# Performance work log

Measured on AMD Instinct MI355X. Metric: run time of the kernel, lower is better.

## Reference

```python
import jax, jax.numpy as jnp
import numpy as np

IN_C, OUT_C, K, STRIDE, PAD, N_EXPERTS = 64, 128, 3, 1, 1, 4
B, H, W = 32, 64, 64


def setup_inputs() -> dict:
    key = jax.random.key(0)
    k1, k2, k3, k4 = jax.random.split(key, 4)
    x = jax.random.normal(k1, (B, IN_C, H, W), dtype=jnp.float32)
    idx = jax.random.randint(k2, (B,), 0, N_EXPERTS, dtype=jnp.int64)
    # Expert conv weights/biases (PyTorch Conv2d layout: [out_c, in_c, kh, kw])
    fan_in = IN_C * K * K
    bound = 1.0 / np.sqrt(fan_in)
    Wc = jax.random.uniform(k3, (N_EXPERTS, OUT_C, IN_C, K, K), dtype=jnp.float32,
                            minval=-bound, maxval=bound)
    bc = jax.random.uniform(k4, (N_EXPERTS, OUT_C), dtype=jnp.float32,
                            minval=-bound, maxval=bound)
    return {"x": x, "idx": idx, "Wc": Wc, "bc": bc}


def _conv2d(x, w, b):
    # x: [B, C_in, H, W], w: [C_out, C_in, K, K], b: [C_out]
    y = jax.lax.conv_general_dilated(
        x, w,
        window_strides=(STRIDE, STRIDE),
        padding=[(PAD, PAD), (PAD, PAD)],
        dimension_numbers=("NCHW", "OIHW", "NCHW"),
    )
    return y + b[None, :, None, None]


def reference(x, idx, Wc, bc):
    # Compute every expert's conv for every sample (faithful to the torch code),
    # then gather each sample's selected expert output.
    results = jax.vmap(lambda w, b: _conv2d(x, w, b))(Wc, bc)  # [E, B, C_out, H, W]
    results = jnp.moveaxis(results, 0, 1)                      # [B, E, C_out, H, W]
    out = jnp.take_along_axis(
        results, idx[:, None, None, None, None].astype(jnp.int32), axis=1
    )  # [B, 1, C_out, H, W]
    return jnp.squeeze(out, axis=1)
```

## Files before the change

### kernel.cpp

```cpp
#include <hip/hip_runtime.h>
#include <hip/hip_bf16.h>


#define IC 64
#define OC 128
#define HH 64
#define WW 64

typedef short short8 __attribute__((ext_vector_type(8)));
typedef ushort ushort8 __attribute__((ext_vector_type(8)));
typedef float float16 __attribute__((ext_vector_type(16)));

typedef const __attribute__((address_space(1))) void gas_t;
typedef __attribute__((address_space(3))) void las_t;

static __device__ __forceinline__ ushort f2bf(float v) {
    __hip_bfloat16 h = __float2bfloat16(v);
    return *(ushort*)&h;
}

__global__ __launch_bounds__(256)
void reorder_w(const float* __restrict__ Wc, ushort* __restrict__ wout) {
    __shared__ ushort lw[4 * 584];
    const int t   = threadIdx.x;
    const int e   = blockIdx.x >> 5;
    const int oc0 = (blockIdx.x & 31) * 4;
    const float* src = Wc + (size_t)(e * 128 + oc0) * 576;
#pragma unroll
    for (int k = 0; k < 9; ++k) {
        const int f   = k * 256 + t;
        const int ocl = f / 576;
        const int rem = f - ocl * 576;
        lw[ocl * 584 + rem] = f2bf(src[f]);
    }
    __syncthreads();
#pragma unroll
    for (int k = 0; k < 2; ++k) {
        const int n = k * 256 + t;
        if (n < 288) {
            const int ocl = n & 3, ich = (n >> 2) & 7, tap = n >> 5;
            ushort8 v;
#pragma unroll
            for (int icl = 0; icl < 8; ++icl)
                v[icl] = lw[ocl * 584 + (ich * 8 + icl) * 9 + tap];
            *(ushort8*)(wout +
                ((((size_t)(e * 9 + tap) * 8 + ich) * 128 + oc0 + ocl) * 8)) = v;
        }
    }
}

__global__ __launch_bounds__(256, 4)
void moe_conv_mfma(const float* __restrict__ x, const int* __restrict__ idx,
                   const ushort* __restrict__ wre, const float* __restrict__ bc,
                   float* __restrict__ out) {
    __shared__ __align__(16) ushort xs[4 * 8 * 66 * 8];
    __shared__ __align__(16) ushort wbuf[2][8192];
    __shared__ float bias[128];

    const int t = threadIdx.x;

    const int lin = blockIdx.x;
    const int nw  = (lin & 7) * 128 + (lin >> 3);
    const int b   = nw >> 5;
    const int rp  = nw & 31;
    const int row0 = rp * 2;
    const int e    = ((unsigned)idx[b]) & 3;

    const int lane31 = t & 31;
    const int lane64 = t & 63;
    const int lhi    = (t >> 5) & 1;
    const int wv     = t >> 6;
    const int w0     = wv & 1;
    const int pr     = wv >> 1;

    const ushort* we = wre + (size_t)e * 9 * 8192;

#pragma unroll
    for (int i = 0; i < 4; ++i) {
        __builtin_amdgcn_global_load_lds(
            (gas_t*)(we + wv * 2048 + i * 512 + lane64 * 8),
            (las_t*)&wbuf[0][wv * 2048 + i * 512], 16, 0, 0);
    }

    if (t < 128) {
        const int r = t >> 5, rem = t & 31;
        const int ich = rem >> 2, side = (rem >> 1) & 1, q = rem & 1;
        const int hc = side ? 65 : 0;
        ushort4 z = {0, 0, 0, 0};
        *(ushort4*)&xs[(((r * 8 + ich) * 66 + hc) * 8 + q * 4)] = z;
    } else {
        bias[t - 128] = bc[e * OC + (t - 128)];
    }

    const float* xb = x + (size_t)b * IC * HH * WW;
    {
        const int gc   = t & 63;
        const int csel = t >> 6;
#pragma unroll
        for (int it = 0; it < 16; ++it) {
            const int combo = it * 4 + csel;
            const int r = combo >> 4, rem = combo & 15;
            const int ich = rem >> 1, q = rem & 1;
            const int gr = row0 - 1 + r;
            ushort4 u = {0, 0, 0, 0};
            if ((unsigned)gr < (unsigned)HH) {
                const int ic0 = ich * 8 + q * 4;
                u.x = f2bf(xb[((ic0 + 0) * HH + gr) * WW + gc]);
                u.y = f2bf(xb[((ic0 + 1) * HH + gr) * WW + gc]);
                u.z = f2bf(xb[((ic0 + 2) * HH + gr) * WW + gc]);
                u.w = f2bf(xb[((ic0 + 3) * HH + gr) * WW + gc]);
            }
            *(ushort4*)&xs[(((r * 8 + ich) * 66 + (gc + 1)) * 8 + q * 4)] = u;
        }
    }

    float16 acc[2][2];
#pragma unroll
    for (int a = 0; a < 2; ++a)
#pragma unroll
        for (int cg = 0; cg < 2; ++cg)
#pragma unroll
            for (int r = 0; r < 16; ++r) acc[a][cg][r] = 0.0f;

    const int xbase = ((pr * 8 + lhi) * 66 + lane31) * 8;

#pragma unroll
    for (int tap = 0; tap < 9; ++tap) {
        const int cur = tap & 1;
        if (tap < 8) {
            const ushort* wt = we + (tap + 1) * 8192;
#pragma unroll
            for (int i = 0; i < 4; ++i) {
                __builtin_amdgcn_global_load_lds(
                    (gas_t*)(wt + wv * 2048 + i * 512 + lane64 * 8),
                    (las_t*)&wbuf[cur ^ 1][wv * 2048 + i * 512], 16, 0, 0);
            }
            asm volatile("s_waitcnt vmcnt(4) lgkmcnt(0)" ::: "memory");
        } else {
            asm volatile("s_waitcnt vmcnt(0) lgkmcnt(0)" ::: "memory");
        }
        __builtin_amdgcn_s_barrier();

        const int kh = tap / 3;
        const int kw = tap - kh * 3;
        const int off = ((kh * 8) * 66 + kw) * 8;

        __builtin_amdgcn_s_setprio(1);
#pragma unroll
        for (int ks = 0; ks < 4; ++ks) {
            const int ich = ks * 2 + lhi;
            const short8 a0 = *(const short8*)&wbuf[cur][(ich * 128 + w0 * 64 + lane31) * 8];
            const short8 a1 = *(const short8*)&wbuf[cur][(ich * 128 + w0 * 64 + 32 + lane31) * 8];
            const short8 b0 = *(const short8*)&xs[xbase + off + ks * 2 * 66 * 8];
            const short8 b1 = *(const short8*)&xs[xbase + off + ks * 2 * 66 * 8 + 256];
            acc[0][0] = __builtin_amdgcn_mfma_f32_32x32x16_bf16(a0, b0, acc[0][0], 0, 0, 0);
            acc[0][1] = __builtin_amdgcn_mfma_f32_32x32x16_bf16(a0, b1, acc[0][1], 0, 0, 0);
            acc[1][0] = __builtin_amdgcn_mfma_f32_32x32x16_bf16(a1, b0, acc[1][0], 0, 0, 0);
            acc[1][1] = __builtin_amdgcn_mfma_f32_32x32x16_bf16(a1, b1, acc[1][1], 0, 0, 0);
        }
        __builtin_amdgcn_s_setprio(0);

        __builtin_amdgcn_s_barrier();
    }

#pragma unroll
    for (int a = 0; a < 2; ++a) {
        const int ocb = w0 * 64 + a * 32 + 4 * lhi;
#pragma unroll
        for (int reg = 0; reg < 16; ++reg) {
            const int oc = ocb + (reg & 3) + 8 * (reg >> 2);
            const float bv = bias[oc];
            const size_t base = (((size_t)b * OC + oc) * HH + (row0 + pr)) * WW;
            out[base + lane31]      = acc[a][0][reg] + bv;
            out[base + 32 + lane31] = acc[a][1][reg] + bv;
        }
    }
}

extern "C" void kernel_launch(void* const* d_in, const int* in_sizes, int n_in,
                              void* d_out, int out_size, void* d_ws, size_t ws_size,
                              hipStream_t stream) {
    const float* x   = (const float*)d_in[0];
    const int*   idx = (const int*)d_in[1];
    const float* Wc  = (const float*)d_in[2];
    const float* bc  = (const float*)d_in[3];
    float* out  = (float*)d_out;
    ushort* wre = (ushort*)d_ws;

    reorder_w<<<128, 256, 0, stream>>>(Wc, wre);
    moe_conv_mfma<<<1024, 256, 0, stream>>>(x, idx, wre, bc, out);
}
```

Baseline: 120.0 us.

## Enlarge conv tile to 8 output rows per 512-thread block with full OC per wave

Each block now computes 8 output rows with 8 waves, each wave covering all 128 output channels for one row, instead of 2 rows with 4 waves splitting the channels. The input halo shrinks relative to useful rows (10 staged rows for 8 outputs instead of 4 for 2), and each weight tap loaded into LDS is reused across four times as many output rows. This cuts redundant x loads and bf16 conversion as well as weight traffic. In exchange it doubles accumulator registers per wave, uses more LDS, and launches only 256 blocks, which lowers occupancy and may underfill the GPU's CUs.

```diff
diff --git a/kernel.cpp b/kernel.cpp
--- a/kernel.cpp
+++ b/kernel.cpp
@@ -49,47 +49,44 @@
     }
 }
 
-__global__ __launch_bounds__(256, 4)
+__global__ __launch_bounds__(512, 2)
 void moe_conv_mfma(const float* __restrict__ x, const int* __restrict__ idx,
                    const ushort* __restrict__ wre, const float* __restrict__ bc,
                    float* __restrict__ out) {
-    __shared__ __align__(16) ushort xs[4 * 8 * 66 * 8];
+    __shared__ __align__(16) ushort xs[10 * 8 * 66 * 8];
     __shared__ __align__(16) ushort wbuf[2][8192];
     __shared__ float bias[128];
 
     const int t = threadIdx.x;
 
     const int lin = blockIdx.x;
-    const int nw  = (lin & 7) * 128 + (lin >> 3);
-    const int b   = nw >> 5;
-    const int rp  = nw & 31;
-    const int row0 = rp * 2;
+    const int nw  = (lin & 7) * 32 + (lin >> 3);
+    const int b   = nw >> 3;
+    const int rq  = nw & 7;
+    const int row0 = rq * 8;
     const int e    = ((unsigned)idx[b]) & 3;
 
     const int lane31 = t & 31;
-    const int lane64 = t & 63;
     const int lhi    = (t >> 5) & 1;
     const int wv     = t >> 6;
-    const int w0     = wv & 1;
-    const int pr     = wv >> 1;
 
     const ushort* we = wre + (size_t)e * 9 * 8192;
 
 #pragma unroll
-    for (int i = 0; i < 4; ++i) {
+    for (int i = 0; i < 2; ++i) {
         __builtin_amdgcn_global_load_lds(
-            (gas_t*)(we + wv * 2048 + i * 512 + lane64 * 8),
-            (las_t*)&wbuf[0][wv * 2048 + i * 512], 16, 0, 0);
+            (gas_t*)(we + i * 4096 + t * 8),
+            (las_t*)&wbuf[0][i * 4096 + t * 8], 16, 0, 0);
     }
 
-    if (t < 128) {
+    if (t < 320) {
         const int r = t >> 5, rem = t & 31;
         const int ich = rem >> 2, side = (rem >> 1) & 1, q = rem & 1;
         const int hc = side ? 65 : 0;
         ushort4 z = {0, 0, 0, 0};
         *(ushort4*)&xs[(((r * 8 + ich) * 66 + hc) * 8 + q * 4)] = z;
-    } else {
-        bias[t - 128] = bc[e * OC + (t - 128)];
+    } else if (t < 448) {
+        bias[t - 320] = bc[e * OC + (t - 320)];
     }
 
     const float* xb = x + (size_t)b * IC * HH * WW;
@@ -97,8 +94,8 @@
         const int gc   = t & 63;
         const int csel = t >> 6;
 #pragma unroll
-        for (int it = 0; it < 16; ++it) {
-            const int combo = it * 4 + csel;
+        for (int it = 0; it < 20; ++it) {
+            const int combo = it * 8 + csel;
             const int r = combo >> 4, rem = combo & 15;
             const int ich = rem >> 1, q = rem & 1;
             const int gr = row0 - 1 + r;
@@ -114,15 +111,16 @@
         }
     }
 
-    float16 acc[2][2];
+    float16 acc[4][2];
 #pragma unroll
-    for (int a = 0; a < 2; ++a)
+    for (int g = 0; g < 4; ++g)
 #pragma unroll
         for (int cg = 0; cg < 2; ++cg)
 #pragma unroll
-            for (int r = 0; r < 16; ++r) acc[a][cg][r] = 0.0f;
+            for (int r = 0; r < 16; ++r) acc[g][cg][r] = 0.0f;
 
-    const int xbase = ((pr * 8 + lhi) * 66 + lane31) * 8;
+    const int xrow  = wv * 4224 + lane31 * 8;
+    const int abase = lane31 * 8;
 
 #pragma unroll
     for (int tap = 0; tap < 9; ++tap) {
@@ -130,12 +128,12 @@
         if (tap < 8) {
             const ushort* wt = we + (tap + 1) * 8192;
 #pragma unroll
-            for (int i = 0; i < 4; ++i) {
+            for (int i = 0; i < 2; ++i) {
                 __builtin_amdgcn_global_load_lds(
-                    (gas_t*)(wt + wv * 2048 + i * 512 + lane64 * 8),
-                    (las_t*)&wbuf[cur ^ 1][wv * 2048 + i * 512], 16, 0, 0);
+                    (gas_t*)(wt + i * 4096 + t * 8),
+                    (las_t*)&wbuf[cur ^ 1][i * 4096 + t * 8], 16, 0, 0);
             }
-            asm volatile("s_waitcnt vmcnt(4) lgkmcnt(0)" ::: "memory");
+            asm volatile("s_waitcnt vmcnt(2) lgkmcnt(0)" ::: "memory");
         } else {
             asm volatile("s_waitcnt vmcnt(0) lgkmcnt(0)" ::: "memory");
         }
@@ -143,36 +141,45 @@
 
         const int kh = tap / 3;
         const int kw = tap - kh * 3;
-        const int off = ((kh * 8) * 66 + kw) * 8;
+        const int xtap = xrow + kh * 4224 + kw * 8;
 
         __builtin_amdgcn_s_setprio(1);
 #pragma unroll
         for (int ks = 0; ks < 4; ++ks) {
             const int ich = ks * 2 + lhi;
-            const short8 a0 = *(const short8*)&wbuf[cur][(ich * 128 + w0 * 64 + lane31) * 8];
-            const short8 a1 = *(const short8*)&wbuf[cur][(ich * 128 + w0 * 64 + 32 + lane31) * 8];
-            const short8 b0 = *(const short8*)&xs[xbase + off + ks * 2 * 66 * 8];
-            const short8 b1 = *(const short8*)&xs[xbase + off + ks * 2 * 66 * 8 + 256];
+            const int xo = xtap + ich * 528;
+            const short8 b0 = *(const short8*)&xs[xo];
+            const short8 b1 = *(const short8*)&xs[xo + 256];
+            const int ao = abase + ich * 1024;
+            const short8 a0 = *(const short8*)&wbuf[cur][ao];
+            const short8 a1 = *(const short8*)&wbuf[cur][ao + 256];
+            const short8 a2 = *(const short8*)&wbuf[cur][ao + 512];
+            const short8 a3 = *(const short8*)&wbuf[cur][ao + 768];
             acc[0][0] = __builtin_amdgcn_mfma_f32_32x32x16_bf16(a0, b0, acc[0][0], 0, 0, 0);
             acc[0][1] = __builtin_amdgcn_mfma_f32_32x32x16_bf16(a0, b1, acc[0][1], 0, 0, 0);
             acc[1][0] = __builtin_amdgcn_mfma_f32_32x32x16_bf16(a1, b0, acc[1][0], 0, 0, 0);
             acc[1][1] = __builtin_amdgcn_mfma_f32_32x32x16_bf16(a1, b1, acc[1][1], 0, 0, 0);
+            acc[2][0] = __builtin_amdgcn_mfma_f32_32x32x16_bf16(a2, b0, acc[2][0], 0, 0, 0);
+            acc[2][1] = __builtin_amdgcn_mfma_f32_32x32x16_bf16(a2, b1, acc[2][1], 0, 0, 0);
+            acc[3][0] = __builtin_amdgcn_mfma_f32_32x32x16_bf16(a3, b0, acc[3][0], 0, 0, 0);
+            acc[3][1] = __builtin_amdgcn_mfma_f32_32x32x16_bf16(a3, b1, acc[3][1], 0, 0, 0);
         }
         __builtin_amdgcn_s_setprio(0);
 
-        __builtin_amdgcn_s_barrier();
+        if (tap < 8)
+            __builtin_amdgcn_s_barrier();
     }
 
 #pragma unroll
-    for (int a = 0; a < 2; ++a) {
-        const int ocb = w0 * 64 + a * 32 + 4 * lhi;
+    for (int g = 0; g < 4; ++g) {
+        const int ocb = g * 32 + 4 * lhi;
 #pragma unroll
         for (int reg = 0; reg < 16; ++reg) {
             const int oc = ocb + (reg & 3) + 8 * (reg >> 2);
             const float bv = bias[oc];
-            const size_t base = (((size_t)b * OC + oc) * HH + (row0 + pr)) * WW;
-            out[base + lane31]      = acc[a][0][reg] + bv;
-            out[base + 32 + lane31] = acc[a][1][reg] + bv;
+            const size_t base = (((size_t)b * OC + oc) * HH + (row0 + wv)) * WW;
+            out[base + lane31]      = acc[g][0][reg] + bv;
+            out[base + 32 + lane31] = acc[g][1][reg] + bv;
         }
     }
 }
@@ -188,5 +195,5 @@
     ushort* wre = (ushort*)d_ws;
 
     reorder_w<<<128, 256, 0, stream>>>(Wc, wre);
-    moe_conv_mfma<<<1024, 256, 0, stream>>>(x, idx, wre, bc, out);
+    moe_conv_mfma<<<256, 512, 0, stream>>>(x, idx, wre, bc, out);
 }
```

After: 112.2 us. 6.5% less time.

## Enlarge conv tile to four output rows per 512-thread block, single-buffer weights

Applied to the files above, without the earlier changes.

Each block now computes four output rows with eight waves instead of two rows with four waves. This cuts redundant input-halo loads and halves per-row weight fetches. The weight buffer becomes single-buffered, with the next tap's load issued after the compute barrier, to keep LDS use about the same despite the larger input tile. The cost is losing overlap between weight loads and MFMA work within a block.

```diff
diff --git a/kernel.cpp b/kernel.cpp
--- a/kernel.cpp
+++ b/kernel.cpp
@@ -49,25 +49,24 @@
     }
 }
 
-__global__ __launch_bounds__(256, 4)
+__global__ __launch_bounds__(512, 4)
 void moe_conv_mfma(const float* __restrict__ x, const int* __restrict__ idx,
                    const ushort* __restrict__ wre, const float* __restrict__ bc,
                    float* __restrict__ out) {
-    __shared__ __align__(16) ushort xs[4 * 8 * 66 * 8];
-    __shared__ __align__(16) ushort wbuf[2][8192];
+    __shared__ __align__(16) ushort xs[6 * 8 * 66 * 8];
+    __shared__ __align__(16) ushort wbuf[8192];
     __shared__ float bias[128];
 
     const int t = threadIdx.x;
 
     const int lin = blockIdx.x;
-    const int nw  = (lin & 7) * 128 + (lin >> 3);
-    const int b   = nw >> 5;
-    const int rp  = nw & 31;
-    const int row0 = rp * 2;
+    const int nw  = (lin & 7) * 64 + (lin >> 3);
+    const int b   = nw >> 4;
+    const int rq  = nw & 15;
+    const int row0 = rq * 4;
     const int e    = ((unsigned)idx[b]) & 3;
 
     const int lane31 = t & 31;
-    const int lane64 = t & 63;
     const int lhi    = (t >> 5) & 1;
     const int wv     = t >> 6;
     const int w0     = wv & 1;
@@ -76,20 +75,20 @@
     const ushort* we = wre + (size_t)e * 9 * 8192;
 
 #pragma unroll
-    for (int i = 0; i < 4; ++i) {
+    for (int i = 0; i < 2; ++i) {
         __builtin_amdgcn_global_load_lds(
-            (gas_t*)(we + wv * 2048 + i * 512 + lane64 * 8),
-            (las_t*)&wbuf[0][wv * 2048 + i * 512], 16, 0, 0);
+            (gas_t*)(we + i * 4096 + t * 8),
+            (las_t*)&wbuf[i * 4096 + t * 8], 16, 0, 0);
     }
 
-    if (t < 128) {
+    if (t < 192) {
         const int r = t >> 5, rem = t & 31;
         const int ich = rem >> 2, side = (rem >> 1) & 1, q = rem & 1;
         const int hc = side ? 65 : 0;
         ushort4 z = {0, 0, 0, 0};
         *(ushort4*)&xs[(((r * 8 + ich) * 66 + hc) * 8 + q * 4)] = z;
-    } else {
-        bias[t - 128] = bc[e * OC + (t - 128)];
+    } else if (t < 320) {
+        bias[t - 192] = bc[e * OC + (t - 192)];
     }
 
     const float* xb = x + (size_t)b * IC * HH * WW;
@@ -97,8 +96,8 @@
         const int gc   = t & 63;
         const int csel = t >> 6;
 #pragma unroll
-        for (int it = 0; it < 16; ++it) {
-            const int combo = it * 4 + csel;
+        for (int it = 0; it < 12; ++it) {
+            const int combo = it * 8 + csel;
             const int r = combo >> 4, rem = combo & 15;
             const int ich = rem >> 1, q = rem & 1;
             const int gr = row0 - 1 + r;
@@ -122,37 +121,24 @@
 #pragma unroll
             for (int r = 0; r < 16; ++r) acc[a][cg][r] = 0.0f;
 
-    const int xbase = ((pr * 8 + lhi) * 66 + lane31) * 8;
-
 #pragma unroll
     for (int tap = 0; tap < 9; ++tap) {
-        const int cur = tap & 1;
-        if (tap < 8) {
-            const ushort* wt = we + (tap + 1) * 8192;
-#pragma unroll
-            for (int i = 0; i < 4; ++i) {
-                __builtin_amdgcn_global_load_lds(
-                    (gas_t*)(wt + wv * 2048 + i * 512 + lane64 * 8),
-                    (las_t*)&wbuf[cur ^ 1][wv * 2048 + i * 512], 16, 0, 0);
-            }
-            asm volatile("s_waitcnt vmcnt(4) lgkmcnt(0)" ::: "memory");
-        } else {
-            asm volatile("s_waitcnt vmcnt(0) lgkmcnt(0)" ::: "memory");
-        }
+        asm volatile("s_waitcnt vmcnt(0) lgkmcnt(0)" ::: "memory");
         __builtin_amdgcn_s_barrier();
 
         const int kh = tap / 3;
         const int kw = tap - kh * 3;
-        const int off = ((kh * 8) * 66 + kw) * 8;
+        const int rr = pr + kh;
+        const int hb = lane31 + kw;
 
         __builtin_amdgcn_s_setprio(1);
 #pragma unroll
         for (int ks = 0; ks < 4; ++ks) {
             const int ich = ks * 2 + lhi;
-            const short8 a0 = *(const short8*)&wbuf[cur][(ich * 128 + w0 * 64 + lane31) * 8];
-            const short8 a1 = *(const short8*)&wbuf[cur][(ich * 128 + w0 * 64 + 32 + lane31) * 8];
-            const short8 b0 = *(const short8*)&xs[xbase + off + ks * 2 * 66 * 8];
-            const short8 b1 = *(const short8*)&xs[xbase + off + ks * 2 * 66 * 8 + 256];
+            const short8 a0 = *(const short8*)&wbuf[(ich * 128 + w0 * 64 + lane31) * 8];
+            const short8 a1 = *(const short8*)&wbuf[(ich * 128 + w0 * 64 + 32 + lane31) * 8];
+            const short8 b0 = *(const short8*)&xs[((rr * 8 + ich) * 66 + hb) * 8];
+            const short8 b1 = *(const short8*)&xs[((rr * 8 + ich) * 66 + hb + 32) * 8];
             acc[0][0] = __builtin_amdgcn_mfma_f32_32x32x16_bf16(a0, b0, acc[0][0], 0, 0, 0);
             acc[0][1] = __builtin_amdgcn_mfma_f32_32x32x16_bf16(a0, b1, acc[0][1], 0, 0, 0);
             acc[1][0] = __builtin_amdgcn_mfma_f32_32x32x16_bf16(a1, b0, acc[1][0], 0, 0, 0);
@@ -161,6 +147,15 @@
         __builtin_amdgcn_s_setprio(0);
 
         __builtin_amdgcn_s_barrier();
+        if (tap < 8) {
+            const ushort* wt = we + (tap + 1) * 8192;
+#pragma unroll
+            for (int i = 0; i < 2; ++i) {
+                __builtin_amdgcn_global_load_lds(
+                    (gas_t*)(wt + i * 4096 + t * 8),
+                    (las_t*)&wbuf[i * 4096 + t * 8], 16, 0, 0);
+            }
+        }
     }
 
 #pragma unroll
@@ -188,5 +183,5 @@
     ushort* wre = (ushort*)d_ws;
 
     reorder_w<<<128, 256, 0, stream>>>(Wc, wre);
-    moe_conv_mfma<<<1024, 256, 0, stream>>>(x, idx, wre, bc, out);
+    moe_conv_mfma<<<512, 512, 0, stream>>>(x, idx, wre, bc, out);
 }
```

Result: faster. 112.0 us (-6.7%).
